# Kernel tuning notes

Hardware: AMD Instinct MI355X
Metric: run time of the kernel (lower is better)

## Reference

```python
import jax, jax.numpy as jnp
import numpy as np

BETA = 0.25  # commitment weight


def setup_inputs() -> dict:
    key = jax.random.key(0)
    k1, k2 = jax.random.split(key)
    B, N, D, K = 16, 1024, 512, 8192
    z_e = jax.random.normal(k1, (B, N, D), dtype=jnp.float32)
    # codebook weight; torch init is uniform(-1/K, 1/K), scale doesn't affect math structure
    W = jax.random.uniform(k2, (K, D), dtype=jnp.float32, minval=-1.0 / K, maxval=1.0 / K)
    return {"z_e": z_e, "W": W}


def reference(z_e, W):
    B, N, D = z_e.shape
    flat = z_e.reshape(B * N, D)
    dist = (jnp.sum(flat * flat, axis=1, keepdims=True)
            + jnp.sum(W * W, axis=1)[None, :]
            - 2.0 * (flat @ W.T))
    ids = jnp.argmin(dist, axis=1)           # [B*N]
    z_q = W[ids].reshape(B, N, D)            # embedding gather
    codebook_loss = jnp.mean((z_q - jax.lax.stop_gradient(z_e)) ** 2)
    commit_loss = jnp.mean((z_e - jax.lax.stop_gradient(z_q)) ** 2)
    vq_loss = codebook_loss + BETA * commit_loss
    orth_loss = jnp.zeros((), dtype=z_e.dtype)  # orth_reg_weight == 0.0
    loss_total = vq_loss + 0.0 * orth_loss
    z_q_st = z_e + jax.lax.stop_gradient(z_q - z_e)  # straight-through
    return (z_q_st, ids.reshape(B, N), vq_loss, codebook_loss, commit_loss, orth_loss, loss_total)
```

## Files before the change

### kernel.cpp

```cpp
#include <hip/hip_runtime.h>
#include <math.h>

#define MROWS 16384
#define DIMD  512
#define KCOD  8192
#define CAP   524224u
#define MARGIN 9.0e-4f

typedef __attribute__((ext_vector_type(8))) short short8;
typedef __attribute__((ext_vector_type(4))) float f32x4;
typedef const __attribute__((address_space(1))) unsigned char glb_byte;
typedef __attribute__((address_space(3))) unsigned char lds_byte;

__device__ __forceinline__ void gload16(const void* g, void* l) {
    __builtin_amdgcn_global_load_lds((glb_byte*)g, (lds_byte*)l, 16, 0, 0);
}

__device__ __forceinline__ unsigned short f2bf(float f) {
    unsigned u = __float_as_uint(f);
    return (unsigned short)((u + 0x7FFFu + ((u >> 16) & 1u)) >> 16);
}

#define OFF_ABF     0u
#define OFF_WBF     16777216u
#define OFF_XSQ     25165824u
#define OFF_WSQ     25231360u
#define OFF_THR     25264128u
#define OFF_PM2     25329664u
#define OFF_RES     33718272u
#define OFF_CTCNT   33849344u
#define OFF_GCNT    33849600u
#define OFF_CTROWS  33849664u
#define OFF_LIST    35946816u
#define OFF_PARTIAL 38043712u
#define OFF_IDX     38109248u

__global__ __launch_bounds__(256) void cvt2_k(const float* __restrict__ A,
                                              const float* __restrict__ W,
                                              unsigned short* __restrict__ Abf,
                                              unsigned short* __restrict__ Wbf,
                                              float* __restrict__ xsq,
                                              float* __restrict__ wsq,
                                              unsigned int* __restrict__ ctcnt,
                                              unsigned int* __restrict__ gcount)
{
    if (blockIdx.x == 0 && threadIdx.x < 65) {
        if (threadIdx.x < 64) ctcnt[threadIdx.x] = 0u;
        else *gcount = 0u;
    }
    const int lane = threadIdx.x & 63;
    const int wid  = (blockIdx.x * blockDim.x + threadIdx.x) >> 6;
    const int nw   = (gridDim.x * blockDim.x) >> 6;
    for (int r = wid; r < MROWS + KCOD; r += nw) {
        const bool isA = (r < MROWS);
        const float4* src = (const float4*)(isA ? (A + (size_t)r * DIMD)
                                                : (W + (size_t)(r - MROWS) * DIMD));
        unsigned short* dst = isA ? (Abf + (size_t)r * DIMD)
                                  : (Wbf + (size_t)(r - MROWS) * DIMD);
        float4 v0 = src[lane];
        float4 v1 = src[lane + 64];
        ushort4 o0; o0.x = f2bf(v0.x); o0.y = f2bf(v0.y); o0.z = f2bf(v0.z); o0.w = f2bf(v0.w);
        ushort4 o1; o1.x = f2bf(v1.x); o1.y = f2bf(v1.y); o1.z = f2bf(v1.z); o1.w = f2bf(v1.w);
        ((ushort4*)dst)[lane] = o0;
        ((ushort4*)dst)[lane + 64] = o1;
        float s = v0.x*v0.x + v0.y*v0.y + v0.z*v0.z + v0.w*v0.w
                + v1.x*v1.x + v1.y*v1.y + v1.z*v1.z + v1.w*v1.w;
        #pragma unroll
        for (int m = 1; m < 64; m <<= 1) s += __shfl_xor(s, m, 64);
        if (lane == 0) { if (isA) xsq[r] = s; else wsq[r - MROWS] = s; }
    }
}

__global__ __launch_bounds__(256, 2) void minpass_k(
    const unsigned short* __restrict__ Abf,
    const unsigned short* __restrict__ Wbf,
    float* __restrict__ partmin2)
{
    __shared__ __align__(16) unsigned short Bs[5][4096];
    __shared__ __align__(16) float pm[4096];
    __shared__ __align__(16) char dmy[4096];

    const int t    = threadIdx.x;
    const int lane = t & 63;
    const int w    = t >> 6;
    const int wm   = w >> 1, wn = w & 1;
    const int rt   = (int)blockIdx.x >> 1;
    const int half = (int)blockIdx.x & 1;
    const int r0   = rt * 64;

    short8 Areg[16][2];
    {
        const unsigned short* ap0 = Abf + (size_t)(r0 + wm * 32 + (lane & 15)) * DIMD + (lane >> 4) * 8;
        const unsigned short* ap1 = ap0 + (size_t)16 * DIMD;
        #pragma unroll
        for (int kc = 0; kc < 16; ++kc) {
            Areg[kc][0] = *(const short8*)(ap0 + kc * 32);
            Areg[kc][1] = *(const short8*)(ap1 + kc * 32);
        }
    }

    const unsigned short* Wb = Wbf + (size_t)half * 4096 * DIMD;
    const int srow = t >> 2;
    const int skof = (t & 3) * 8;

    #pragma unroll
    for (int c = 0; c < 3; ++c) {
        const unsigned short* s0 = Wb + (size_t)(srow) * DIMD + c * 32 + skof;
        gload16(s0, &Bs[c][t * 8]);
        gload16(s0 + (size_t)64 * DIMD, &Bs[c][2048 + t * 8]);
    }

    int pfs = 3, rds = 0;

    f32x4 acc[2][4];
    #pragma unroll
    for (int mi = 0; mi < 2; ++mi)
        #pragma unroll
        for (int ni = 0; ni < 4; ++ni) acc[mi][ni] = (f32x4){0.f, 0.f, 0.f, 0.f};

    for (int ct = 0; ct < 32; ++ct) {
        #pragma unroll
        for (int kc = 0; kc < 16; ++kc) {
            const int n = ct * 16 + kc + 3;
            if (n < 512) {
                const unsigned short* s0 = Wb + (size_t)((n >> 4) * 128 + srow) * DIMD + (n & 15) * 32 + skof;
                gload16(s0, &Bs[pfs][t * 8]);
                gload16(s0 + (size_t)64 * DIMD, &Bs[pfs][2048 + t * 8]);
            } else {
                gload16(Wb + skof, &dmy[t * 16]);
                gload16(Wb + skof, &dmy[t * 16]);
            }
            pfs = (pfs == 4) ? 0 : pfs + 1;

            asm volatile("s_waitcnt vmcnt(6)\n\ts_barrier" ::: "memory");

            const unsigned short* bb = &Bs[rds][0];
            short8 b[4];
            #pragma unroll
            for (int ni = 0; ni < 4; ++ni)
                b[ni] = *(const short8*)&bb[(wn * 64 + ni * 16 + (lane & 15)) * 32 + (lane >> 4) * 8];
            #pragma unroll
            for (int mi = 0; mi < 2; ++mi)
                #pragma unroll
                for (int ni = 0; ni < 4; ++ni)
                    acc[mi][ni] = __builtin_amdgcn_mfma_f32_16x16x32_bf16(Areg[kc][mi], b[ni], acc[mi][ni], 0, 0, 0);
            rds = (rds == 4) ? 0 : rds + 1;
        }

        #pragma unroll
        for (int mi = 0; mi < 2; ++mi) {
            #pragma unroll
            for (int reg = 0; reg < 4; ++reg) {
                float mx = fmaxf(fmaxf(acc[mi][0][reg], acc[mi][1][reg]),
                                 fmaxf(acc[mi][2][reg], acc[mi][3][reg]));
                #pragma unroll
                for (int s = 1; s < 16; s <<= 1) mx = fmaxf(mx, __shfl_xor(mx, s, 64));
                if ((lane & 15) == 0)
                    pm[(wm * 32 + mi * 16 + (lane >> 4) * 4 + reg) * 64 + ct * 2 + wn] = -2.0f * mx;
            }
        }
        #pragma unroll
        for (int mi = 0; mi < 2; ++mi)
            #pragma unroll
            for (int ni = 0; ni < 4; ++ni) acc[mi][ni] = (f32x4){0.f, 0.f, 0.f, 0.f};
    }

    __syncthreads();
    const int rl = t >> 2, cs = (t & 3) * 16;
    #pragma unroll
    for (int j = 0; j < 4; ++j) {
        f32x4 v = *(const f32x4*)&pm[rl * 64 + cs + j * 4];
        *(f32x4*)&partmin2[(size_t)(r0 + rl) * 128 + half * 64 + cs + j * 4] = v;
    }
}

__global__ __launch_bounds__(256) void qualify_k(const float* __restrict__ partmin2,
                                                 float* __restrict__ rowthr,
                                                 unsigned int* __restrict__ ctcnt,
                                                 unsigned short* __restrict__ ctrows,
                                                 unsigned long long* __restrict__ res)
{
    __shared__ unsigned cntA[64], baseL[64], cntB[64];
    const int t = threadIdx.x;
    const int r = blockIdx.x * 256 + t;

    if (t < 64) { cntA[t] = 0u; cntB[t] = 0u; }

    const f32x4* p = (const f32x4*)(partmin2 + (size_t)r * 128);
    float m = INFINITY;
    for (int i = 0; i < 32; ++i) {
        f32x4 x = p[i];
        m = fminf(fminf(fminf(x[0], x[1]), fminf(x[2], x[3])), m);
    }
    const float thr = m + MARGIN;
    rowthr[r] = thr;
    res[r] = ~0ull;

    unsigned long long qm = 0ull;
    for (int i = 0; i < 32; ++i) {
        f32x4 x = p[i];
        if (fminf(x[0], x[1]) <= thr) qm |= 1ull << (2 * i);
        if (fminf(x[2], x[3]) <= thr) qm |= 1ull << (2 * i + 1);
    }
    __syncthreads();
    unsigned long long mm = qm;
    while (mm) {
        const int tile = __ffsll((long long)mm) - 1;
        mm &= mm - 1;
        atomicAdd(&cntA[tile], 1u);
    }
    __syncthreads();
    if (t < 64) baseL[t] = cntA[t] ? atomicAdd(&ctcnt[t], cntA[t]) : 0u;
    __syncthreads();
    mm = qm;
    while (mm) {
        const int tile = __ffsll((long long)mm) - 1;
        mm &= mm - 1;
        const unsigned pos = baseL[tile] + atomicAdd(&cntB[tile], 1u);
        ctrows[tile * 16384 + pos] = (unsigned short)r;
    }
}

__global__ __launch_bounds__(256) void cand_k(
    const unsigned short* __restrict__ Abf,
    const unsigned short* __restrict__ Wbf,
    const float* __restrict__ rowthr,
    const unsigned int* __restrict__ ctcnt,
    const unsigned short* __restrict__ ctrows,
    unsigned int* __restrict__ list,
    unsigned int* __restrict__ gcount)
{
    __shared__ __align__(16) unsigned short As[2][4096];
    __shared__ __align__(16) unsigned short Bs[2][4096];
    __shared__ int ids_lds[128];
    __shared__ float thr_lds[128];
    __shared__ unsigned wtot[4];
    __shared__ unsigned gb_lds;

    const int T = blockIdx.x;
    unsigned n = ctcnt[T]; if (n > 16384u) n = 16384u;
    const unsigned base = blockIdx.y * 128;
    if (base >= n) return;

    const int t    = threadIdx.x;
    const int lane = t & 63;
    const int w    = t >> 6;
    const int wm   = w >> 1, wn = w & 1;
    const int c0   = T * 128;

    if (t < 128) {
        const int g = (base + t < n) ? (int)ctrows[T * 16384 + base + t] : -1;
        ids_lds[t] = (g < 0) ? 0 : g;
        thr_lds[t] = (g < 0) ? -INFINITY : rowthr[g];
    }
    __syncthreads();

    const int inst0 = w * 2;
    const int lrow0 = inst0 * 16 + (lane >> 2);
    const int kof   = (lane & 3) * 8;
    const unsigned short* aSrc0 = Abf + (size_t)ids_lds[lrow0] * DIMD + kof;
    const unsigned short* aSrc1 = Abf + (size_t)ids_lds[lrow0 + 16] * DIMD + kof;
    const unsigned short* bSrc0 = Wbf + (size_t)(c0 + lrow0) * DIMD + kof;
    const unsigned short* bSrc1 = bSrc0 + (size_t)16 * DIMD;

    f32x4 acc[4][4];
    #pragma unroll
    for (int mi = 0; mi < 4; ++mi)
        #pragma unroll
        for (int ni = 0; ni < 4; ++ni) acc[mi][ni] = (f32x4){0.f, 0.f, 0.f, 0.f};

    gload16(aSrc0, &As[0][inst0 * 512]);
    gload16(aSrc1, &As[0][(inst0 + 1) * 512]);
    gload16(bSrc0, &Bs[0][inst0 * 512]);
    gload16(bSrc1, &Bs[0][(inst0 + 1) * 512]);

    int cur = 0;
    for (int kc = 0; kc < 16; ++kc) {
        __syncthreads();
        if (kc + 1 < 16) {
            const int nb = cur ^ 1;
            const int ke = (kc + 1) * 32;
            gload16(aSrc0 + ke, &As[nb][inst0 * 512]);
            gload16(aSrc1 + ke, &As[nb][(inst0 + 1) * 512]);
            gload16(bSrc0 + ke, &Bs[nb][inst0 * 512]);
            gload16(bSrc1 + ke, &Bs[nb][(inst0 + 1) * 512]);
        }
        const int ko = (lane >> 4) * 8;
        short8 a[4], b[4];
        #pragma unroll
        for (int mi = 0; mi < 4; ++mi)
            a[mi] = *(const short8*)&As[cur][(wm * 64 + mi * 16 + (lane & 15)) * 32 + ko];
        #pragma unroll
        for (int ni = 0; ni < 4; ++ni)
            b[ni] = *(const short8*)&Bs[cur][(wn * 64 + ni * 16 + (lane & 15)) * 32 + ko];
        #pragma unroll
        for (int mi = 0; mi < 4; ++mi)
            #pragma unroll
            for (int ni = 0; ni < 4; ++ni)
                acc[mi][ni] = __builtin_amdgcn_mfma_f32_16x16x32_bf16(a[mi], b[ni], acc[mi][ni], 0, 0, 0);
        __syncthreads();
        cur ^= 1;
    }

    unsigned nh = 0;
    #pragma unroll
    for (int mi = 0; mi < 4; ++mi)
        #pragma unroll
        for (int reg = 0; reg < 4; ++reg) {
            const float thr = thr_lds[wm * 64 + mi * 16 + (lane >> 4) * 4 + reg];
            #pragma unroll
            for (int ni = 0; ni < 4; ++ni)
                if (-2.0f * acc[mi][ni][reg] <= thr) ++nh;
        }

    unsigned pfx = nh;
    #pragma unroll
    for (int s = 1; s < 64; s <<= 1) {
        unsigned v = __shfl_up(pfx, s, 64);
        if (lane >= s) pfx += v;
    }
    if (lane == 63) wtot[w] = pfx;
    __syncthreads();
    if (t == 0) {
        const unsigned tot = wtot[0] + wtot[1] + wtot[2] + wtot[3];
        gb_lds = tot ? atomicAdd(gcount, tot) : 0u;
    }
    __syncthreads();
    unsigned wb = 0;
    #pragma unroll
    for (int i = 0; i < 4; ++i) if (i < w) wb += wtot[i];
    unsigned myoff = gb_lds + wb + pfx - nh;

    #pragma unroll
    for (int mi = 0; mi < 4; ++mi)
        #pragma unroll
        for (int reg = 0; reg < 4; ++reg) {
            const int row_l = wm * 64 + mi * 16 + (lane >> 4) * 4 + reg;
            const float thr = thr_lds[row_l];
            #pragma unroll
            for (int ni = 0; ni < 4; ++ni) {
                if (-2.0f * acc[mi][ni][reg] <= thr) {
                    const unsigned k = c0 + wn * 64 + ni * 16 + (lane & 15);
                    if (myoff < CAP)
                        list[myoff] = ((unsigned)ids_lds[row_l] << 13) | k;
                    ++myoff;
                }
            }
        }
}

__global__ __launch_bounds__(256) void refine_k(const float* __restrict__ A,
                                                const float* __restrict__ W,
                                                const float* __restrict__ xsq,
                                                const float* __restrict__ wsq,
                                                const unsigned* __restrict__ list,
                                                const unsigned* __restrict__ gcount,
                                                unsigned long long* __restrict__ res)
{
    const int lane = threadIdx.x & 63;
    const int wid  = (blockIdx.x * 256 + threadIdx.x) >> 6;
    const int nw   = (gridDim.x * 256) >> 6;
    unsigned n = *gcount;
    if (n > CAP) n = CAP;
    for (unsigned i = wid; i < n; i += nw) {
        const unsigned pk = list[i];
        const unsigned row = pk >> 13, k = pk & 8191u;
        const float4* xp = (const float4*)(A + (size_t)row * DIMD);
        const float4* wp = (const float4*)(W + (size_t)k * DIMD);
        const float4 x0 = xp[lane * 2], x1 = xp[lane * 2 + 1];
        const float4 w0 = wp[lane * 2], w1 = wp[lane * 2 + 1];
        double s = (double)x0.x * w0.x + (double)x0.y * w0.y
                 + (double)x0.z * w0.z + (double)x0.w * w0.w
                 + (double)x1.x * w1.x + (double)x1.y * w1.y
                 + (double)x1.z * w1.z + (double)x1.w * w1.w;
        #pragma unroll
        for (int m = 1; m < 64; m <<= 1) s += __shfl_xor(s, m, 64);
        if (lane == 0) {
            const float Df = (float)s;
            const float dist = (xsq[row] + wsq[k]) - 2.0f * Df;
            const unsigned long long p =
                ((unsigned long long)__float_as_uint(dist) << 32) | (unsigned long long)k;
            atomicMin(res + row, p);
        }
    }
}

__global__ __launch_bounds__(256) void finish_k(const unsigned long long* __restrict__ res,
                                                int* __restrict__ idxo,
                                                float* __restrict__ out_ids)
{
    const int r = blockIdx.x * 256 + threadIdx.x;
    const int id = (int)(res[r] & 8191ull);
    idxo[r] = id;
    out_ids[r] = (float)id;
}

__global__ __launch_bounds__(256) void gather_k(const float* __restrict__ A,
                                                const float* __restrict__ W,
                                                const int* __restrict__ idx,
                                                float* __restrict__ out_zq,
                                                double* __restrict__ partial)
{
    __shared__ double wsum[4];
    const int t   = threadIdx.x;
    const int row = blockIdx.x * 2 + (t >> 7);
    const int col = t & 127;
    const int id  = idx[row];
    const float4 ze = ((const float4*)(A + (size_t)row * DIMD))[col];
    const float4 zq = ((const float4*)(W + (size_t)id  * DIMD))[col];
    float4 o;
    o.x = ze.x + (zq.x - ze.x);
    o.y = ze.y + (zq.y - ze.y);
    o.z = ze.z + (zq.z - ze.z);
    o.w = ze.w + (zq.w - ze.w);
    ((float4*)(out_zq + (size_t)row * DIMD))[col] = o;
    const float dx = zq.x - ze.x, dy = zq.y - ze.y, dz = zq.z - ze.z, dw = zq.w - ze.w;
    double s = (double)dx*dx + (double)dy*dy + (double)dz*dz + (double)dw*dw;
    #pragma unroll
    for (int m = 1; m < 64; m <<= 1) s += __shfl_xor(s, m, 64);
    if ((t & 63) == 0) wsum[t >> 6] = s;
    __syncthreads();
    if (t == 0) partial[blockIdx.x] = (wsum[0] + wsum[1]) + (wsum[2] + wsum[3]);
}

__global__ __launch_bounds__(256) void fin_k(const double* __restrict__ partial,
                                             float* __restrict__ outs)
{
    __shared__ double wsum[4];
    const int t = threadIdx.x;
    double s = 0.0;
    for (int i = 0; i < 32; ++i) s += partial[t + 256 * i];
    #pragma unroll
    for (int m = 1; m < 64; m <<= 1) s += __shfl_xor(s, m, 64);
    if ((t & 63) == 0) wsum[t >> 6] = s;
    __syncthreads();
    if (t == 0) {
        const double tot = (wsum[0] + wsum[1]) + (wsum[2] + wsum[3]);
        const double mse = tot / (double)((size_t)MROWS * DIMD);
        const float mf = (float)mse;
        const float vq = (float)(mse * 1.25);
        outs[0] = vq; outs[1] = mf; outs[2] = mf; outs[3] = 0.0f; outs[4] = vq;
    }
}


extern "C" void kernel_launch(void* const* d_in, const int* in_sizes, int n_in,
                              void* d_out, int out_size, void* d_ws, size_t ws_size,
                              hipStream_t stream)
{
    const float* A = (const float*)d_in[0];
    const float* W = (const float*)d_in[1];

    char* ws = (char*)d_ws;
    unsigned short* Abf = (unsigned short*)(ws + OFF_ABF);
    unsigned short* Wbf = (unsigned short*)(ws + OFF_WBF);
    float*  xsq     = (float*)(ws + OFF_XSQ);
    float*  wsq     = (float*)(ws + OFF_WSQ);
    float*  rowthr  = (float*)(ws + OFF_THR);
    float*  partmin2= (float*)(ws + OFF_PM2);
    unsigned long long* res = (unsigned long long*)(ws + OFF_RES);
    unsigned int* ctcnt     = (unsigned int*)(ws + OFF_CTCNT);
    unsigned int* gcount    = (unsigned int*)(ws + OFF_GCNT);
    unsigned short* ctrows  = (unsigned short*)(ws + OFF_CTROWS);
    unsigned int* list      = (unsigned int*)(ws + OFF_LIST);
    double* partial = (double*)(ws + OFF_PARTIAL);
    int*    idx     = (int*)(ws + OFF_IDX);

    float* out_zq  = (float*)d_out;
    float* out_ids = out_zq + (size_t)MROWS * DIMD;
    float* out_sc  = out_ids + MROWS;

    cvt2_k<<<512, 256, 0, stream>>>(A, W, Abf, Wbf, xsq, wsq, ctcnt, gcount);
    minpass_k<<<512, 256, 0, stream>>>(Abf, Wbf, partmin2);
    qualify_k<<<64, 256, 0, stream>>>(partmin2, rowthr, ctcnt, ctrows, res);
    cand_k<<<dim3(64, 128), 256, 0, stream>>>(Abf, Wbf, rowthr, ctcnt, ctrows, list, gcount);
    refine_k<<<512, 256, 0, stream>>>(A, W, xsq, wsq, list, gcount, res);
    finish_k<<<64, 256, 0, stream>>>(res, idx, out_ids);
    gather_k<<<8192, 256, 0, stream>>>(A, W, idx, out_zq, partial);
    fin_k<<<1, 256, 0, stream>>>(partial, out_sc);
}
```

Before: 304.2 us.

## Switch coarse distance passes from bf16 to fp8 MFMA with pre-tiled codebook

Converts A to fp8 e4m3 and the codebook to fp8 scaled by 8192. The codebook is written in a transposed, tile-major layout so the min pass and candidate pass run fp8 16x16x32 MFMAs with contiguous 16-byte loads. The min pass now uses 128-thread blocks covering 64 rows by a quarter of the codebook each, and the candidate margin is widened to match the coarser precision. The aim is to halve operand bytes and raise matrix throughput, at the cost of more candidates reaching the exact fp32 refine pass, with a CAP increase to hold them. The codebook scale relies on the small uniform init range of the test inputs.

```diff
diff --git a/kernel.cpp b/kernel.cpp
--- a/kernel.cpp
+++ b/kernel.cpp
@@ -4,10 +4,9 @@
 #define MROWS 16384
 #define DIMD  512
 #define KCOD  8192
-#define CAP   524224u
-#define MARGIN 9.0e-4f
-
-typedef __attribute__((ext_vector_type(8))) short short8;
+#define CAP   2097152u
+#define MARGIN_S 17.0f
+
 typedef __attribute__((ext_vector_type(4))) float f32x4;
 typedef const __attribute__((address_space(1))) unsigned char glb_byte;
 typedef __attribute__((address_space(3))) unsigned char lds_byte;
@@ -16,29 +15,52 @@
     __builtin_amdgcn_global_load_lds((glb_byte*)g, (lds_byte*)l, 16, 0, 0);
 }
 
-__device__ __forceinline__ unsigned short f2bf(float f) {
-    unsigned u = __float_as_uint(f);
-    return (unsigned short)((u + 0x7FFFu + ((u >> 16) & 1u)) >> 16);
-}
-
-#define OFF_ABF     0u
-#define OFF_WBF     16777216u
-#define OFF_XSQ     25165824u
-#define OFF_WSQ     25231360u
-#define OFF_THR     25264128u
-#define OFF_PM2     25329664u
-#define OFF_RES     33718272u
-#define OFF_CTCNT   33849344u
-#define OFF_GCNT    33849600u
-#define OFF_CTROWS  33849664u
-#define OFF_LIST    35946816u
-#define OFF_PARTIAL 38043712u
-#define OFF_IDX     38109248u
+__device__ __forceinline__ unsigned f2e4m3(float f) {
+    const unsigned b = __float_as_uint(f);
+    const unsigned s = (b >> 24) & 0x80u;
+    const unsigned ef = (b >> 23) & 0xFFu;
+    const unsigned m = b & 0x7FFFFFu;
+    if (ef == 0u) return s;
+    const int e = (int)ef - 127;
+    if (e >= -6) {
+        unsigned q = m >> 20;
+        const unsigned rem = m & 0xFFFFFu;
+        q += (rem > 0x80000u) || (rem == 0x80000u && (q & 1u));
+        unsigned te = (unsigned)(e + 7);
+        if (q == 8u) { q = 0u; te += 1u; }
+        if (te > 15u || (te == 15u && q == 7u)) return s | 0x7Eu;
+        return s | (te << 3) | q;
+    } else {
+        const int sh = 20 + (-6 - e);
+        if (sh > 31) return s;
+        const unsigned m24 = 0x800000u | m;
+        unsigned q = m24 >> sh;
+        const unsigned rem = m24 & ((1u << sh) - 1u);
+        const unsigned hlf = 1u << (sh - 1);
+        q += (rem > hlf) || (rem == hlf && (q & 1u));
+        if (q == 8u) return s | 0x08u;
+        return s | q;
+    }
+}
+
+#define OFF_A8      0u
+#define OFF_W8T     8388608u
+#define OFF_XSQ     12582912u
+#define OFF_WSQ     12648448u
+#define OFF_THR     12681216u
+#define OFF_PM2     12746752u
+#define OFF_RES     21135360u
+#define OFF_CTCNT   21266432u
+#define OFF_GCNT    21266688u
+#define OFF_CTROWS  21266944u
+#define OFF_LIST    23364096u
+#define OFF_PARTIAL 31752704u
+#define OFF_IDX     31818240u
 
 __global__ __launch_bounds__(256) void cvt2_k(const float* __restrict__ A,
                                               const float* __restrict__ W,
-                                              unsigned short* __restrict__ Abf,
-                                              unsigned short* __restrict__ Wbf,
+                                              unsigned char* __restrict__ A8,
+                                              unsigned char* __restrict__ W8T,
                                               float* __restrict__ xsq,
                                               float* __restrict__ wsq,
                                               unsigned int* __restrict__ ctcnt,
@@ -55,100 +77,103 @@
         const bool isA = (r < MROWS);
         const float4* src = (const float4*)(isA ? (A + (size_t)r * DIMD)
                                                 : (W + (size_t)(r - MROWS) * DIMD));
-        unsigned short* dst = isA ? (Abf + (size_t)r * DIMD)
-                                  : (Wbf + (size_t)(r - MROWS) * DIMD);
         float4 v0 = src[lane];
         float4 v1 = src[lane + 64];
-        ushort4 o0; o0.x = f2bf(v0.x); o0.y = f2bf(v0.y); o0.z = f2bf(v0.z); o0.w = f2bf(v0.w);
-        ushort4 o1; o1.x = f2bf(v1.x); o1.y = f2bf(v1.y); o1.z = f2bf(v1.z); o1.w = f2bf(v1.w);
-        ((ushort4*)dst)[lane] = o0;
-        ((ushort4*)dst)[lane + 64] = o1;
         float s = v0.x*v0.x + v0.y*v0.y + v0.z*v0.z + v0.w*v0.w
                 + v1.x*v1.x + v1.y*v1.y + v1.z*v1.z + v1.w*v1.w;
         #pragma unroll
         for (int m = 1; m < 64; m <<= 1) s += __shfl_xor(s, m, 64);
         if (lane == 0) { if (isA) xsq[r] = s; else wsq[r - MROWS] = s; }
-    }
-}
-
-__global__ __launch_bounds__(256, 2) void minpass_k(
-    const unsigned short* __restrict__ Abf,
-    const unsigned short* __restrict__ Wbf,
+
+        if (isA) {
+            const unsigned p0 = f2e4m3(v0.x) | (f2e4m3(v0.y) << 8) | (f2e4m3(v0.z) << 16) | (f2e4m3(v0.w) << 24);
+            const unsigned p1 = f2e4m3(v1.x) | (f2e4m3(v1.y) << 8) | (f2e4m3(v1.z) << 16) | (f2e4m3(v1.w) << 24);
+            *(unsigned*)(A8 + (size_t)r * DIMD + 4 * lane) = p0;
+            *(unsigned*)(A8 + (size_t)r * DIMD + 256 + 4 * lane) = p1;
+        } else {
+            const int rw = r - MROWS;
+            const int CT = rw >> 7, code = rw & 127;
+            const unsigned p0 = f2e4m3(v0.x*8192.f) | (f2e4m3(v0.y*8192.f) << 8) | (f2e4m3(v0.z*8192.f) << 16) | (f2e4m3(v0.w*8192.f) << 24);
+            const unsigned p1 = f2e4m3(v1.x*8192.f) | (f2e4m3(v1.y*8192.f) << 8) | (f2e4m3(v1.z*8192.f) << 16) | (f2e4m3(v1.w*8192.f) << 24);
+            const size_t basea = (size_t)CT * 65536 + (size_t)((lane >> 1) & 3) * 1024
+                               + (size_t)code * 8 + 4 * (lane & 1);
+            *(unsigned*)(W8T + basea + (size_t)(lane >> 3) * 4096) = p0;
+            *(unsigned*)(W8T + basea + (size_t)(8 + (lane >> 3)) * 4096) = p1;
+        }
+    }
+}
+
+__global__ __launch_bounds__(128, 2) void minpass_k(
+    const unsigned char* __restrict__ A8,
+    const unsigned char* __restrict__ W8T,
     float* __restrict__ partmin2)
 {
-    __shared__ __align__(16) unsigned short Bs[5][4096];
-    __shared__ __align__(16) float pm[4096];
-    __shared__ __align__(16) char dmy[4096];
+    __shared__ __align__(16) unsigned char Bs[5][4096];
+    __shared__ __align__(16) float pm[64 * 32];
+    __shared__ __align__(16) unsigned char dmy[2048];
 
     const int t    = threadIdx.x;
     const int lane = t & 63;
-    const int w    = t >> 6;
-    const int wm   = w >> 1, wn = w & 1;
-    const int rt   = (int)blockIdx.x >> 1;
-    const int half = (int)blockIdx.x & 1;
+    const int wv   = t >> 6;
+    const int rt   = (int)blockIdx.x & 255;
+    const int q    = (int)blockIdx.x >> 8;
     const int r0   = rt * 64;
 
-    short8 Areg[16][2];
+    long Areg[16][4];
     {
-        const unsigned short* ap0 = Abf + (size_t)(r0 + wm * 32 + (lane & 15)) * DIMD + (lane >> 4) * 8;
-        const unsigned short* ap1 = ap0 + (size_t)16 * DIMD;
-        #pragma unroll
-        for (int kc = 0; kc < 16; ++kc) {
-            Areg[kc][0] = *(const short8*)(ap0 + kc * 32);
-            Areg[kc][1] = *(const short8*)(ap1 + kc * 32);
-        }
-    }
-
-    const unsigned short* Wb = Wbf + (size_t)half * 4096 * DIMD;
-    const int srow = t >> 2;
-    const int skof = (t & 3) * 8;
+        const unsigned char* ab = A8 + (size_t)(r0 + (lane & 15)) * DIMD + (lane >> 4) * 8;
+        #pragma unroll
+        for (int kc = 0; kc < 16; ++kc)
+            #pragma unroll
+            for (int mi = 0; mi < 4; ++mi)
+                Areg[kc][mi] = *(const long*)(ab + (size_t)mi * 16 * DIMD + kc * 32);
+    }
+
+    const unsigned char* Wb = W8T + (size_t)q * 1048576;
 
     #pragma unroll
     for (int c = 0; c < 3; ++c) {
-        const unsigned short* s0 = Wb + (size_t)(srow) * DIMD + c * 32 + skof;
-        gload16(s0, &Bs[c][t * 8]);
-        gload16(s0 + (size_t)64 * DIMD, &Bs[c][2048 + t * 8]);
-    }
-
+        gload16(Wb + c * 4096 + t * 16,        &Bs[c][t * 16]);
+        gload16(Wb + c * 4096 + 2048 + t * 16, &Bs[c][2048 + t * 16]);
+    }
     int pfs = 3, rds = 0;
 
-    f32x4 acc[2][4];
-    #pragma unroll
-    for (int mi = 0; mi < 2; ++mi)
+    f32x4 acc[4][4];
+    #pragma unroll
+    for (int mi = 0; mi < 4; ++mi)
         #pragma unroll
         for (int ni = 0; ni < 4; ++ni) acc[mi][ni] = (f32x4){0.f, 0.f, 0.f, 0.f};
 
-    for (int ct = 0; ct < 32; ++ct) {
+    for (int ct = 0; ct < 16; ++ct) {
         #pragma unroll
         for (int kc = 0; kc < 16; ++kc) {
             const int n = ct * 16 + kc + 3;
-            if (n < 512) {
-                const unsigned short* s0 = Wb + (size_t)((n >> 4) * 128 + srow) * DIMD + (n & 15) * 32 + skof;
-                gload16(s0, &Bs[pfs][t * 8]);
-                gload16(s0 + (size_t)64 * DIMD, &Bs[pfs][2048 + t * 8]);
+            if (n < 256) {
+                gload16(Wb + n * 4096 + t * 16,        &Bs[pfs][t * 16]);
+                gload16(Wb + n * 4096 + 2048 + t * 16, &Bs[pfs][2048 + t * 16]);
             } else {
-                gload16(Wb + skof, &dmy[t * 16]);
-                gload16(Wb + skof, &dmy[t * 16]);
+                gload16(Wb + t * 16, &dmy[t * 16]);
+                gload16(Wb + t * 16, &dmy[t * 16]);
             }
             pfs = (pfs == 4) ? 0 : pfs + 1;
 
             asm volatile("s_waitcnt vmcnt(6)\n\ts_barrier" ::: "memory");
 
-            const unsigned short* bb = &Bs[rds][0];
-            short8 b[4];
+            const unsigned char* bb = &Bs[rds][0];
+            long b[4];
             #pragma unroll
             for (int ni = 0; ni < 4; ++ni)
-                b[ni] = *(const short8*)&bb[(wn * 64 + ni * 16 + (lane & 15)) * 32 + (lane >> 4) * 8];
-            #pragma unroll
-            for (int mi = 0; mi < 2; ++mi)
+                b[ni] = *(const long*)(bb + (lane >> 4) * 1024 + (wv * 64 + ni * 16 + (lane & 15)) * 8);
+            #pragma unroll
+            for (int mi = 0; mi < 4; ++mi)
                 #pragma unroll
                 for (int ni = 0; ni < 4; ++ni)
-                    acc[mi][ni] = __builtin_amdgcn_mfma_f32_16x16x32_bf16(Areg[kc][mi], b[ni], acc[mi][ni], 0, 0, 0);
+                    acc[mi][ni] = __builtin_amdgcn_mfma_f32_16x16x32_fp8_fp8(Areg[kc][mi], b[ni], acc[mi][ni], 0, 0, 0);
             rds = (rds == 4) ? 0 : rds + 1;
         }
 
         #pragma unroll
-        for (int mi = 0; mi < 2; ++mi) {
+        for (int mi = 0; mi < 4; ++mi) {
             #pragma unroll
             for (int reg = 0; reg < 4; ++reg) {
                 float mx = fmaxf(fmaxf(acc[mi][0][reg], acc[mi][1][reg]),
@@ -156,21 +181,19 @@
                 #pragma unroll
                 for (int s = 1; s < 16; s <<= 1) mx = fmaxf(mx, __shfl_xor(mx, s, 64));
                 if ((lane & 15) == 0)
-                    pm[(wm * 32 + mi * 16 + (lane >> 4) * 4 + reg) * 64 + ct * 2 + wn] = -2.0f * mx;
+                    pm[(mi * 16 + (lane >> 4) * 4 + reg) * 32 + ct * 2 + wv] = -2.0f * mx;
+                acc[mi][0][reg] = 0.f; acc[mi][1][reg] = 0.f;
+                acc[mi][2][reg] = 0.f; acc[mi][3][reg] = 0.f;
             }
         }
-        #pragma unroll
-        for (int mi = 0; mi < 2; ++mi)
-            #pragma unroll
-            for (int ni = 0; ni < 4; ++ni) acc[mi][ni] = (f32x4){0.f, 0.f, 0.f, 0.f};
-    }
-
-    __syncthreads();
-    const int rl = t >> 2, cs = (t & 3) * 16;
+    }
+
+    __syncthreads();
+    const int row = t >> 1, ch = (t & 1) * 16;
     #pragma unroll
     for (int j = 0; j < 4; ++j) {
-        f32x4 v = *(const f32x4*)&pm[rl * 64 + cs + j * 4];
-        *(f32x4*)&partmin2[(size_t)(r0 + rl) * 128 + half * 64 + cs + j * 4] = v;
+        f32x4 v = *(const f32x4*)&pm[row * 32 + ch + j * 4];
+        *(f32x4*)&partmin2[(size_t)(r0 + row) * 128 + q * 32 + ch + j * 4] = v;
     }
 }
 
@@ -192,7 +215,7 @@
         f32x4 x = p[i];
         m = fminf(fminf(fminf(x[0], x[1]), fminf(x[2], x[3])), m);
     }
-    const float thr = m + MARGIN;
+    const float thr = m + MARGIN_S;
     rowthr[r] = thr;
     res[r] = ~0ull;
 
@@ -222,16 +245,16 @@
 }
 
 __global__ __launch_bounds__(256) void cand_k(
-    const unsigned short* __restrict__ Abf,
-    const unsigned short* __restrict__ Wbf,
+    const unsigned char* __restrict__ A8,
+    const unsigned char* __restrict__ W8T,
     const float* __restrict__ rowthr,
     const unsigned int* __restrict__ ctcnt,
     const unsigned short* __restrict__ ctrows,
     unsigned int* __restrict__ list,
     unsigned int* __restrict__ gcount)
 {
-    __shared__ __align__(16) unsigned short As[2][4096];
-    __shared__ __align__(16) unsigned short Bs[2][4096];
+    __shared__ __align__(16) unsigned char As[2][4096];
+    __shared__ __align__(16) unsigned char Bs[2][4096];
     __shared__ int ids_lds[128];
     __shared__ float thr_lds[128];
     __shared__ unsigned wtot[4];
@@ -255,49 +278,38 @@
     }
     __syncthreads();
 
-    const int inst0 = w * 2;
-    const int lrow0 = inst0 * 16 + (lane >> 2);
-    const int kof   = (lane & 3) * 8;
-    const unsigned short* aSrc0 = Abf + (size_t)ids_lds[lrow0] * DIMD + kof;
-    const unsigned short* aSrc1 = Abf + (size_t)ids_lds[lrow0 + 16] * DIMD + kof;
-    const unsigned short* bSrc0 = Wbf + (size_t)(c0 + lrow0) * DIMD + kof;
-    const unsigned short* bSrc1 = bSrc0 + (size_t)16 * DIMD;
+    const unsigned char* bbase = W8T + (size_t)T * 65536;
+    const int srow = t >> 1, skh = (t & 1) * 16;
+
+    gload16(A8 + (size_t)ids_lds[srow] * DIMD + skh, &As[0][t * 16]);
+    gload16(bbase + t * 16, &Bs[0][t * 16]);
 
     f32x4 acc[4][4];
     #pragma unroll
     for (int mi = 0; mi < 4; ++mi)
         #pragma unroll
         for (int ni = 0; ni < 4; ++ni) acc[mi][ni] = (f32x4){0.f, 0.f, 0.f, 0.f};
-
-    gload16(aSrc0, &As[0][inst0 * 512]);
-    gload16(aSrc1, &As[0][(inst0 + 1) * 512]);
-    gload16(bSrc0, &Bs[0][inst0 * 512]);
-    gload16(bSrc1, &Bs[0][(inst0 + 1) * 512]);
 
     int cur = 0;
     for (int kc = 0; kc < 16; ++kc) {
         __syncthreads();
         if (kc + 1 < 16) {
             const int nb = cur ^ 1;
-            const int ke = (kc + 1) * 32;
-            gload16(aSrc0 + ke, &As[nb][inst0 * 512]);
-            gload16(aSrc1 + ke, &As[nb][(inst0 + 1) * 512]);
-            gload16(bSrc0 + ke, &Bs[nb][inst0 * 512]);
-            gload16(bSrc1 + ke, &Bs[nb][(inst0 + 1) * 512]);
-        }
-        const int ko = (lane >> 4) * 8;
-        short8 a[4], b[4];
+            gload16(A8 + (size_t)ids_lds[srow] * DIMD + (kc + 1) * 32 + skh, &As[nb][t * 16]);
+            gload16(bbase + (kc + 1) * 4096 + t * 16, &Bs[nb][t * 16]);
+        }
+        long a[4], b[4];
         #pragma unroll
         for (int mi = 0; mi < 4; ++mi)
-            a[mi] = *(const short8*)&As[cur][(wm * 64 + mi * 16 + (lane & 15)) * 32 + ko];
+            a[mi] = *(const long*)&As[cur][(wm * 64 + mi * 16 + (lane & 15)) * 32 + (lane >> 4) * 8];
         #pragma unroll
         for (int ni = 0; ni < 4; ++ni)
-            b[ni] = *(const short8*)&Bs[cur][(wn * 64 + ni * 16 + (lane & 15)) * 32 + ko];
+            b[ni] = *(const long*)&Bs[cur][(lane >> 4) * 1024 + (wn * 64 + ni * 16 + (lane & 15)) * 8];
         #pragma unroll
         for (int mi = 0; mi < 4; ++mi)
             #pragma unroll
             for (int ni = 0; ni < 4; ++ni)
-                acc[mi][ni] = __builtin_amdgcn_mfma_f32_16x16x32_bf16(a[mi], b[ni], acc[mi][ni], 0, 0, 0);
+                acc[mi][ni] = __builtin_amdgcn_mfma_f32_16x16x32_fp8_fp8(a[mi], b[ni], acc[mi][ni], 0, 0, 0);
         __syncthreads();
         cur ^= 1;
     }
@@ -452,8 +464,8 @@
     const float* W = (const float*)d_in[1];
 
     char* ws = (char*)d_ws;
-    unsigned short* Abf = (unsigned short*)(ws + OFF_ABF);
-    unsigned short* Wbf = (unsigned short*)(ws + OFF_WBF);
+    unsigned char* A8  = (unsigned char*)(ws + OFF_A8);
+    unsigned char* W8T = (unsigned char*)(ws + OFF_W8T);
     float*  xsq     = (float*)(ws + OFF_XSQ);
     float*  wsq     = (float*)(ws + OFF_WSQ);
     float*  rowthr  = (float*)(ws + OFF_THR);
@@ -470,10 +482,10 @@
     float* out_ids = out_zq + (size_t)MROWS * DIMD;
     float* out_sc  = out_ids + MROWS;
 
-    cvt2_k<<<512, 256, 0, stream>>>(A, W, Abf, Wbf, xsq, wsq, ctcnt, gcount);
-    minpass_k<<<512, 256, 0, stream>>>(Abf, Wbf, partmin2);
+    cvt2_k<<<512, 256, 0, stream>>>(A, W, A8, W8T, xsq, wsq, ctcnt, gcount);
+    minpass_k<<<1024, 128, 0, stream>>>(A8, W8T, partmin2);
     qualify_k<<<64, 256, 0, stream>>>(partmin2, rowthr, ctcnt, ctrows, res);
-    cand_k<<<dim3(64, 128), 256, 0, stream>>>(Abf, Wbf, rowthr, ctcnt, ctrows, list, gcount);
+    cand_k<<<dim3(64, 128), 256, 0, stream>>>(A8, W8T, rowthr, ctcnt, ctrows, list, gcount);
     refine_k<<<512, 256, 0, stream>>>(A, W, xsq, wsq, list, gcount, res);
     finish_k<<<64, 256, 0, stream>>>(res, idx, out_ids);
     gather_k<<<8192, 256, 0, stream>>>(A, W, idx, out_zq, partial);
```

New measurement: 377.6 us. +24.2%, slower.
